# Optimization experiments

Measured on AMD Instinct MI355X. Metric: run time of the kernel, lower is better.

The kernel has to match this reference:

```python
import jax, jax.numpy as jnp
import numpy as np

N_NODES = 100_000
N_EDGES = 3_200_000
D_FEAT = 64


def setup_inputs() -> dict:
    key = jax.random.key(0)
    k1, k2, k3, k4, k5 = jax.random.split(key, 5)
    x = jax.random.normal(k1, (N_EDGES, D_FEAT), dtype=jnp.float32)
    switch = jax.random.uniform(k2, (N_EDGES,), dtype=jnp.float32)
    edge_src = jax.random.randint(k3, (N_EDGES,), 0, N_NODES, dtype=jnp.int32)
    edge_dst = jax.random.randint(k4, (N_EDGES,), 0, N_NODES, dtype=jnp.int32)
    species = jax.random.randint(k5, (N_NODES,), 0, 90, dtype=jnp.int32)
    return {"x": x, "switch": switch, "edge_src": edge_src,
            "edge_dst": edge_dst, "species": species}


def reference(x, switch, edge_src, edge_dst, species):
    # nat = inputs['species'].shape[0]  (static under jit)
    nat = species.shape[0]
    # apply_switch: gate each edge feature row by its scalar switch value
    xg = x * switch[:, None]                      # [E, D]
    # undirected graph: scatter-add into both endpoints
    out = jax.ops.segment_sum(xg, edge_src, num_segments=nat)
    out = out + jax.ops.segment_sum(xg, edge_dst, num_segments=nat)
    return out                                     # [nat, D]
```

## Files before the change

### kernel.cpp

```cpp
#include <hip/hip_runtime.h>


#define D_FEAT 64
#define EPB 8192
#define KMAX 1024
#define BCAP 24576

__global__ __launch_bounds__(256) void scatter_edges_atomic_kernel(
    const float4* __restrict__ x, const float* __restrict__ sw,
    const int* __restrict__ src, const int* __restrict__ dst,
    float* __restrict__ out, int n_edges)
{
    long long tid = (long long)blockIdx.x * blockDim.x + threadIdx.x;
    long long total = (long long)n_edges * 16;
    if (tid >= total) return;
    int e = (int)(tid >> 4);
    int q = (int)(tid & 15);
    float s = sw[e];
    float4 v = x[(long long)e * 16 + q];
    v.x *= s; v.y *= s; v.z *= s; v.w *= s;
    float* oa = out + (long long)src[e] * D_FEAT + q * 4;
    float* ob = out + (long long)dst[e] * D_FEAT + q * 4;
    unsafeAtomicAdd(oa + 0, v.x); unsafeAtomicAdd(oa + 1, v.y);
    unsafeAtomicAdd(oa + 2, v.z); unsafeAtomicAdd(oa + 3, v.w);
    unsafeAtomicAdd(ob + 0, v.x); unsafeAtomicAdd(ob + 1, v.y);
    unsafeAtomicAdd(ob + 2, v.z); unsafeAtomicAdd(ob + 3, v.w);
}

__global__ __launch_bounds__(512) void bucket_hist_kernel(
    const int* __restrict__ src, const int* __restrict__ dst,
    int* __restrict__ bsize, int n_edges, int K)
{
    __shared__ int h[KMAX];
    for (int j = threadIdx.x; j < K; j += 512) h[j] = 0;
    __syncthreads();
    int base = blockIdx.x * EPB;
    int m = min(EPB, n_edges - base);
    for (int i = threadIdx.x; i < m; i += 512) {
        int s = src[base + i], d = dst[base + i];
        atomicAdd(&h[s >> 8], 1);
        atomicAdd(&h[d >> 8], 1);
    }
    __syncthreads();
    for (int j = threadIdx.x; j < K; j += 512)
        if (h[j]) atomicAdd(&bsize[j], h[j]);
}

__global__ __launch_bounds__(1024) void bucket_scan_kernel(
    const int* __restrict__ bsize, int* __restrict__ bbase,
    int* __restrict__ bcursor, int K)
{
    __shared__ int s[KMAX + 1];
    int t = threadIdx.x;
    if (t < K) s[t] = bsize[t];
    __syncthreads();
    if (t == 0) {
        int a = 0;
        for (int j = 0; j < K; ++j) { int v = s[j]; s[j] = a; a += v; }
        s[K] = a;
    }
    __syncthreads();
    if (t <= K) bbase[t] = s[t];
    if (t < K)  bcursor[t] = s[t];
}

__global__ __launch_bounds__(512) void partition_kernel(
    const int* __restrict__ src, const int* __restrict__ dst,
    int* __restrict__ bcursor, unsigned int* __restrict__ pe, int n_edges)
{
    __shared__ int ebs[EPB];
    __shared__ int ebd[EPB];
    __shared__ int cnt[KMAX];
    __shared__ int cur[KMAX];
    for (int j = threadIdx.x; j < KMAX; j += 512) cnt[j] = 0;
    __syncthreads();
    int base = blockIdx.x * EPB;
    int m = min(EPB, n_edges - base);
    for (int i = threadIdx.x; i < m; i += 512) {
        int s = src[base + i], d = dst[base + i];
        ebs[i] = s; ebd[i] = d;
        atomicAdd(&cnt[s >> 8], 1);
        atomicAdd(&cnt[d >> 8], 1);
    }
    __syncthreads();
    for (int j = threadIdx.x; j < KMAX; j += 512) {
        int c = cnt[j];
        cur[j] = c ? atomicAdd(&bcursor[j], c) : 0;
    }
    __syncthreads();
    for (int i = threadIdx.x; i < m; i += 512) {
        unsigned int e = (unsigned int)(base + i);
        int s = ebs[i], d = ebd[i];
        int ps = atomicAdd(&cur[s >> 8], 1);
        pe[ps] = ((unsigned int)(s & 255) << 24) | e;
        int pd = atomicAdd(&cur[d >> 8], 1);
        pe[pd] = ((unsigned int)(d & 255) << 24) | e;
    }
}

__global__ __launch_bounds__(512) void bucket_sort_kernel(
    const int* __restrict__ bbase, unsigned int* __restrict__ pe,
    int* __restrict__ offs_g, int* __restrict__ counts_g, int n_nodes)
{
    __shared__ unsigned int ent[BCAP];
    __shared__ int cnt[256];
    __shared__ int cur[256];
    int k = blockIdx.x;
    int base = bbase[k];
    int m = bbase[k + 1] - base;
    for (int j = threadIdx.x; j < 256; j += 512) cnt[j] = 0;
    __syncthreads();
    for (int i = threadIdx.x; i < m; i += 512) {
        unsigned int v = pe[base + i];
        ent[i] = v;
        atomicAdd(&cnt[v >> 24], 1);
    }
    __syncthreads();
    if (threadIdx.x == 0) {
        int a = 0;
        for (int j = 0; j < 256; ++j) { int c = cnt[j]; cur[j] = a; a += c; }
    }
    __syncthreads();
    for (int j = threadIdx.x; j < 256; j += 512) {
        int lo = cur[j];
        int n = (k << 8) + j;
        if (n < n_nodes) { counts_g[n] = cnt[j]; offs_g[n] = base + lo; }
        cur[j] = base + lo;
    }
    __syncthreads();
    for (int i = threadIdx.x; i < m; i += 512) {
        unsigned int v = ent[i];
        int pos = atomicAdd(&cur[v >> 24], 1);
        pe[pos] = v;
    }
}

__global__ __launch_bounds__(256) void gather_kernel(
    const float* __restrict__ x, const float* __restrict__ sw,
    const int* __restrict__ offs_g, const int* __restrict__ counts_g,
    const unsigned int* __restrict__ pe, float* __restrict__ out, int n_nodes)
{
    int wave = blockIdx.x * 4 + (threadIdx.x >> 6);
    int lane = threadIdx.x & 63;
    if (wave >= n_nodes) return;
    int start = offs_g[wave];
    int cnt = counts_g[wave];

    float acc = 0.0f;
    int i = 0;
    for (; i + 8 <= cnt; i += 8) {
        int e0 = (int)(pe[start + i + 0] & 0x3FFFFFu);
        int e1 = (int)(pe[start + i + 1] & 0x3FFFFFu);
        int e2 = (int)(pe[start + i + 2] & 0x3FFFFFu);
        int e3 = (int)(pe[start + i + 3] & 0x3FFFFFu);
        int e4 = (int)(pe[start + i + 4] & 0x3FFFFFu);
        int e5 = (int)(pe[start + i + 5] & 0x3FFFFFu);
        int e6 = (int)(pe[start + i + 6] & 0x3FFFFFu);
        int e7 = (int)(pe[start + i + 7] & 0x3FFFFFu);
        float v0 = __builtin_nontemporal_load(x + (long long)e0 * D_FEAT + lane);
        float v1 = __builtin_nontemporal_load(x + (long long)e1 * D_FEAT + lane);
        float v2 = __builtin_nontemporal_load(x + (long long)e2 * D_FEAT + lane);
        float v3 = __builtin_nontemporal_load(x + (long long)e3 * D_FEAT + lane);
        float v4 = __builtin_nontemporal_load(x + (long long)e4 * D_FEAT + lane);
        float v5 = __builtin_nontemporal_load(x + (long long)e5 * D_FEAT + lane);
        float v6 = __builtin_nontemporal_load(x + (long long)e6 * D_FEAT + lane);
        float v7 = __builtin_nontemporal_load(x + (long long)e7 * D_FEAT + lane);
        float s0 = sw[e0], s1 = sw[e1], s2 = sw[e2], s3 = sw[e3];
        float s4 = sw[e4], s5 = sw[e5], s6 = sw[e6], s7 = sw[e7];
        acc += v0 * s0; acc += v1 * s1; acc += v2 * s2; acc += v3 * s3;
        acc += v4 * s4; acc += v5 * s5; acc += v6 * s6; acc += v7 * s7;
    }
    for (; i < cnt; ++i) {
        int e = (int)(pe[start + i] & 0x3FFFFFu);
        acc += __builtin_nontemporal_load(x + (long long)e * D_FEAT + lane) * sw[e];
    }
    out[(long long)wave * D_FEAT + lane] = acc;
}

extern "C" void kernel_launch(void* const* d_in, const int* in_sizes, int n_in,
                              void* d_out, int out_size, void* d_ws, size_t ws_size,
                              hipStream_t stream) {
    const float* x   = (const float*)d_in[0];
    const float* sw  = (const float*)d_in[1];
    const int*   src = (const int*)d_in[2];
    const int*   dst = (const int*)d_in[3];
    float* out = (float*)d_out;

    int n_edges = in_sizes[1];
    int n_nodes = in_sizes[4];

    int K = (n_nodes + 255) >> 8;

    char* wsb = (char*)d_ws;
    size_t off = 0;
    int* bsize   = (int*)(wsb + off); off += (size_t)K * 4;
    int* bbase   = (int*)(wsb + off); off += (size_t)(K + 1) * 4;
    int* bcursor = (int*)(wsb + off); off += (size_t)K * 4;
    int* offs_g  = (int*)(wsb + off); off += (size_t)n_nodes * 4;
    int* cnts_g  = (int*)(wsb + off); off += (size_t)n_nodes * 4;
    off = (off + 255) & ~(size_t)255;
    unsigned int* pe = (unsigned int*)(wsb + off);
    off += (size_t)n_edges * 2 * 4;
    size_t needed = off;

    long long avg_per_bucket = (2LL * n_edges) / (K > 0 ? K : 1);
    bool fast_ok = (K >= 1) && (K <= KMAX)
                && (n_edges > 0) && (n_edges < (1 << 22))
                && (avg_per_bucket <= 20000)
                && (ws_size >= needed);

    if (!fast_ok) {
        hipMemsetAsync(d_out, 0, (size_t)out_size * sizeof(float), stream);
        long long total = (long long)n_edges * 16;
        int block = 256;
        long long grid = (total + block - 1) / block;
        scatter_edges_atomic_kernel<<<(int)grid, block, 0, stream>>>(
            (const float4*)x, sw, src, dst, out, n_edges);
        return;
    }

    int nblkE = (n_edges + EPB - 1) / EPB;

    hipMemsetAsync(bsize, 0, (size_t)K * 4, stream);

    bucket_hist_kernel<<<nblkE, 512, 0, stream>>>(src, dst, bsize, n_edges, K);
    bucket_scan_kernel<<<1, 1024, 0, stream>>>(bsize, bbase, bcursor, K);
    partition_kernel<<<nblkE, 512, 0, stream>>>(src, dst, bcursor, pe, n_edges);
    bucket_sort_kernel<<<K, 512, 0, stream>>>(bbase, pe, offs_g, cnts_g, n_nodes);

    int gblk = (n_nodes + 3) / 4;
    gather_kernel<<<gblk, 256, 0, stream>>>(x, sw, offs_g, cnts_g, pe, out, n_nodes);
}
```

Baseline: 477.1 us.

## Use 128-node buckets, parallel scans, and float4 gather with four edges per wave

Bucket size drops from 256 to 128 nodes, so K is 782 and each bucket sort holds fewer entries, which means less shared memory per block and more blocks. The serial single-thread scans in the bucket scan and bucket sort kernels become Hillis-Steele parallel scans. The partition kernel no longer stages src/dst in shared memory and re-reads them from global instead. The gather kernel now processes four edges per wave, each 16-lane group loading a full 256B row as float4 and combining results with xor shuffles. The bucket sort clamps its entry count to BCAP, which could silently drop edges if a bucket overflows.

```diff
diff --git a/kernel.cpp b/kernel.cpp
--- a/kernel.cpp
+++ b/kernel.cpp
@@ -4,7 +4,10 @@
 #define D_FEAT 64
 #define EPB 8192
 #define KMAX 1024
-#define BCAP 24576
+#define BNODES 128
+#define BCAP 12288
+
+typedef float f32x4 __attribute__((ext_vector_type(4)));
 
 __global__ __launch_bounds__(256) void scatter_edges_atomic_kernel(
     const float4* __restrict__ x, const float* __restrict__ sw,
@@ -37,64 +40,63 @@
     int base = blockIdx.x * EPB;
     int m = min(EPB, n_edges - base);
     for (int i = threadIdx.x; i < m; i += 512) {
-        int s = src[base + i], d = dst[base + i];
-        atomicAdd(&h[s >> 8], 1);
-        atomicAdd(&h[d >> 8], 1);
+        atomicAdd(&h[src[base + i] >> 7], 1);
+        atomicAdd(&h[dst[base + i] >> 7], 1);
     }
     __syncthreads();
     for (int j = threadIdx.x; j < K; j += 512)
         if (h[j]) atomicAdd(&bsize[j], h[j]);
 }
 
-__global__ __launch_bounds__(1024) void bucket_scan_kernel(
+__global__ __launch_bounds__(KMAX) void bucket_scan_kernel(
     const int* __restrict__ bsize, int* __restrict__ bbase,
     int* __restrict__ bcursor, int K)
 {
-    __shared__ int s[KMAX + 1];
+    __shared__ int s[KMAX];
     int t = threadIdx.x;
-    if (t < K) s[t] = bsize[t];
-    __syncthreads();
-    if (t == 0) {
-        int a = 0;
-        for (int j = 0; j < K; ++j) { int v = s[j]; s[j] = a; a += v; }
-        s[K] = a;
-    }
-    __syncthreads();
-    if (t <= K) bbase[t] = s[t];
-    if (t < K)  bcursor[t] = s[t];
+    int v = (t < K) ? bsize[t] : 0;
+    int acc = v;
+    s[t] = acc;
+    __syncthreads();
+    for (int d = 1; d < KMAX; d <<= 1) {
+        int add = (t >= d) ? s[t - d] : 0;
+        __syncthreads();
+        acc += add;
+        s[t] = acc;
+        __syncthreads();
+    }
+    if (t < K) { int ex = acc - v; bbase[t] = ex; bcursor[t] = ex; }
+    if (t == K - 1) bbase[K] = acc;
 }
 
 __global__ __launch_bounds__(512) void partition_kernel(
     const int* __restrict__ src, const int* __restrict__ dst,
-    int* __restrict__ bcursor, unsigned int* __restrict__ pe, int n_edges)
-{
-    __shared__ int ebs[EPB];
-    __shared__ int ebd[EPB];
+    int* __restrict__ bcursor, unsigned int* __restrict__ pe,
+    int n_edges, int K)
+{
     __shared__ int cnt[KMAX];
     __shared__ int cur[KMAX];
-    for (int j = threadIdx.x; j < KMAX; j += 512) cnt[j] = 0;
+    for (int j = threadIdx.x; j < K; j += 512) cnt[j] = 0;
     __syncthreads();
     int base = blockIdx.x * EPB;
     int m = min(EPB, n_edges - base);
     for (int i = threadIdx.x; i < m; i += 512) {
-        int s = src[base + i], d = dst[base + i];
-        ebs[i] = s; ebd[i] = d;
-        atomicAdd(&cnt[s >> 8], 1);
-        atomicAdd(&cnt[d >> 8], 1);
-    }
-    __syncthreads();
-    for (int j = threadIdx.x; j < KMAX; j += 512) {
+        atomicAdd(&cnt[src[base + i] >> 7], 1);
+        atomicAdd(&cnt[dst[base + i] >> 7], 1);
+    }
+    __syncthreads();
+    for (int j = threadIdx.x; j < K; j += 512) {
         int c = cnt[j];
         cur[j] = c ? atomicAdd(&bcursor[j], c) : 0;
     }
     __syncthreads();
     for (int i = threadIdx.x; i < m; i += 512) {
+        int s = src[base + i], d = dst[base + i];
         unsigned int e = (unsigned int)(base + i);
-        int s = ebs[i], d = ebd[i];
-        int ps = atomicAdd(&cur[s >> 8], 1);
-        pe[ps] = ((unsigned int)(s & 255) << 24) | e;
-        int pd = atomicAdd(&cur[d >> 8], 1);
-        pe[pd] = ((unsigned int)(d & 255) << 24) | e;
+        int ps = atomicAdd(&cur[s >> 7], 1);
+        pe[ps] = ((unsigned int)(s & 127) << 24) | e;
+        int pd = atomicAdd(&cur[d >> 7], 1);
+        pe[pd] = ((unsigned int)(d & 127) << 24) | e;
     }
 }
 
@@ -103,78 +105,96 @@
     int* __restrict__ offs_g, int* __restrict__ counts_g, int n_nodes)
 {
     __shared__ unsigned int ent[BCAP];
-    __shared__ int cnt[256];
-    __shared__ int cur[256];
+    __shared__ int cnt[BNODES];
+    __shared__ int cur[BNODES];
     int k = blockIdx.x;
+    int t = threadIdx.x;
     int base = bbase[k];
     int m = bbase[k + 1] - base;
-    for (int j = threadIdx.x; j < 256; j += 512) cnt[j] = 0;
-    __syncthreads();
-    for (int i = threadIdx.x; i < m; i += 512) {
+    if (m > BCAP) m = BCAP;
+    if (t < BNODES) cnt[t] = 0;
+    __syncthreads();
+    for (int i = t; i < m; i += 512) {
         unsigned int v = pe[base + i];
         ent[i] = v;
-        atomicAdd(&cnt[v >> 24], 1);
-    }
-    __syncthreads();
-    if (threadIdx.x == 0) {
-        int a = 0;
-        for (int j = 0; j < 256; ++j) { int c = cnt[j]; cur[j] = a; a += c; }
-    }
-    __syncthreads();
-    for (int j = threadIdx.x; j < 256; j += 512) {
-        int lo = cur[j];
-        int n = (k << 8) + j;
-        if (n < n_nodes) { counts_g[n] = cnt[j]; offs_g[n] = base + lo; }
-        cur[j] = base + lo;
-    }
-    __syncthreads();
-    for (int i = threadIdx.x; i < m; i += 512) {
+        atomicAdd(&cnt[(v >> 24) & 127], 1);
+    }
+    __syncthreads();
+    int v0 = 0, acc = 0;
+    if (t < BNODES) { v0 = cnt[t]; acc = v0; cur[t] = acc; }
+    __syncthreads();
+    for (int d = 1; d < BNODES; d <<= 1) {
+        int add = 0;
+        if (t < BNODES && t >= d) add = cur[t - d];
+        __syncthreads();
+        if (t < BNODES) { acc += add; cur[t] = acc; }
+        __syncthreads();
+    }
+    if (t < BNODES) {
+        int ex = acc - v0;
+        int n = (k << 7) + t;
+        if (n < n_nodes) { counts_g[n] = v0; offs_g[n] = base + ex; }
+        cur[t] = base + ex;
+    }
+    __syncthreads();
+    for (int i = t; i < m; i += 512) {
         unsigned int v = ent[i];
-        int pos = atomicAdd(&cur[v >> 24], 1);
+        int pos = atomicAdd(&cur[(v >> 24) & 127], 1);
         pe[pos] = v;
     }
 }
 
 __global__ __launch_bounds__(256) void gather_kernel(
-    const float* __restrict__ x, const float* __restrict__ sw,
+    const f32x4* __restrict__ x4, const float* __restrict__ sw,
     const int* __restrict__ offs_g, const int* __restrict__ counts_g,
-    const unsigned int* __restrict__ pe, float* __restrict__ out, int n_nodes)
+    const unsigned int* __restrict__ pe, f32x4* __restrict__ out4,
+    int n_nodes)
 {
     int wave = blockIdx.x * 4 + (threadIdx.x >> 6);
     int lane = threadIdx.x & 63;
     if (wave >= n_nodes) return;
     int start = offs_g[wave];
     int cnt = counts_g[wave];
-
-    float acc = 0.0f;
+    int cl = lane >> 4;
+    int fq = lane & 15;
+
+    f32x4 acc = {0.f, 0.f, 0.f, 0.f};
     int i = 0;
-    for (; i + 8 <= cnt; i += 8) {
-        int e0 = (int)(pe[start + i + 0] & 0x3FFFFFu);
-        int e1 = (int)(pe[start + i + 1] & 0x3FFFFFu);
-        int e2 = (int)(pe[start + i + 2] & 0x3FFFFFu);
-        int e3 = (int)(pe[start + i + 3] & 0x3FFFFFu);
-        int e4 = (int)(pe[start + i + 4] & 0x3FFFFFu);
-        int e5 = (int)(pe[start + i + 5] & 0x3FFFFFu);
-        int e6 = (int)(pe[start + i + 6] & 0x3FFFFFu);
-        int e7 = (int)(pe[start + i + 7] & 0x3FFFFFu);
-        float v0 = __builtin_nontemporal_load(x + (long long)e0 * D_FEAT + lane);
-        float v1 = __builtin_nontemporal_load(x + (long long)e1 * D_FEAT + lane);
-        float v2 = __builtin_nontemporal_load(x + (long long)e2 * D_FEAT + lane);
-        float v3 = __builtin_nontemporal_load(x + (long long)e3 * D_FEAT + lane);
-        float v4 = __builtin_nontemporal_load(x + (long long)e4 * D_FEAT + lane);
-        float v5 = __builtin_nontemporal_load(x + (long long)e5 * D_FEAT + lane);
-        float v6 = __builtin_nontemporal_load(x + (long long)e6 * D_FEAT + lane);
-        float v7 = __builtin_nontemporal_load(x + (long long)e7 * D_FEAT + lane);
+    for (; i + 16 <= cnt; i += 16) {
+        int j = start + i + cl;
+        unsigned int p0 = pe[j];
+        unsigned int p1 = pe[j + 4];
+        unsigned int p2 = pe[j + 8];
+        unsigned int p3 = pe[j + 12];
+        int e0 = (int)(p0 & 0x3FFFFFu);
+        int e1 = (int)(p1 & 0x3FFFFFu);
+        int e2 = (int)(p2 & 0x3FFFFFu);
+        int e3 = (int)(p3 & 0x3FFFFFu);
+        f32x4 v0 = __builtin_nontemporal_load(x4 + (long long)e0 * 16 + fq);
+        f32x4 v1 = __builtin_nontemporal_load(x4 + (long long)e1 * 16 + fq);
+        f32x4 v2 = __builtin_nontemporal_load(x4 + (long long)e2 * 16 + fq);
+        f32x4 v3 = __builtin_nontemporal_load(x4 + (long long)e3 * 16 + fq);
         float s0 = sw[e0], s1 = sw[e1], s2 = sw[e2], s3 = sw[e3];
-        float s4 = sw[e4], s5 = sw[e5], s6 = sw[e6], s7 = sw[e7];
         acc += v0 * s0; acc += v1 * s1; acc += v2 * s2; acc += v3 * s3;
-        acc += v4 * s4; acc += v5 * s5; acc += v6 * s6; acc += v7 * s7;
-    }
-    for (; i < cnt; ++i) {
-        int e = (int)(pe[start + i] & 0x3FFFFFu);
-        acc += __builtin_nontemporal_load(x + (long long)e * D_FEAT + lane) * sw[e];
-    }
-    out[(long long)wave * D_FEAT + lane] = acc;
+    }
+    for (; i < cnt; i += 4) {
+        int j = i + cl;
+        if (j < cnt) {
+            unsigned int p = pe[start + j];
+            int e = (int)(p & 0x3FFFFFu);
+            f32x4 v = __builtin_nontemporal_load(x4 + (long long)e * 16 + fq);
+            acc += v * sw[e];
+        }
+    }
+    acc.x += __shfl_xor(acc.x, 16, 64);
+    acc.y += __shfl_xor(acc.y, 16, 64);
+    acc.z += __shfl_xor(acc.z, 16, 64);
+    acc.w += __shfl_xor(acc.w, 16, 64);
+    acc.x += __shfl_xor(acc.x, 32, 64);
+    acc.y += __shfl_xor(acc.y, 32, 64);
+    acc.z += __shfl_xor(acc.z, 32, 64);
+    acc.w += __shfl_xor(acc.w, 32, 64);
+    if (cl == 0) out4[(long long)wave * 16 + fq] = acc;
 }
 
 extern "C" void kernel_launch(void* const* d_in, const int* in_sizes, int n_in,
@@ -189,13 +209,14 @@
     int n_edges = in_sizes[1];
     int n_nodes = in_sizes[4];
 
-    int K = (n_nodes + 255) >> 8;
+    int K = (n_nodes + BNODES - 1) >> 7;
 
     char* wsb = (char*)d_ws;
     size_t off = 0;
     int* bsize   = (int*)(wsb + off); off += (size_t)K * 4;
     int* bbase   = (int*)(wsb + off); off += (size_t)(K + 1) * 4;
     int* bcursor = (int*)(wsb + off); off += (size_t)K * 4;
+    off = (off + 255) & ~(size_t)255;
     int* offs_g  = (int*)(wsb + off); off += (size_t)n_nodes * 4;
     int* cnts_g  = (int*)(wsb + off); off += (size_t)n_nodes * 4;
     off = (off + 255) & ~(size_t)255;
@@ -206,7 +227,7 @@
     long long avg_per_bucket = (2LL * n_edges) / (K > 0 ? K : 1);
     bool fast_ok = (K >= 1) && (K <= KMAX)
                 && (n_edges > 0) && (n_edges < (1 << 22))
-                && (avg_per_bucket <= 20000)
+                && (avg_per_bucket <= 10000)
                 && (ws_size >= needed);
 
     if (!fast_ok) {
@@ -224,10 +245,11 @@
     hipMemsetAsync(bsize, 0, (size_t)K * 4, stream);
 
     bucket_hist_kernel<<<nblkE, 512, 0, stream>>>(src, dst, bsize, n_edges, K);
-    bucket_scan_kernel<<<1, 1024, 0, stream>>>(bsize, bbase, bcursor, K);
-    partition_kernel<<<nblkE, 512, 0, stream>>>(src, dst, bcursor, pe, n_edges);
+    bucket_scan_kernel<<<1, KMAX, 0, stream>>>(bsize, bbase, bcursor, K);
+    partition_kernel<<<nblkE, 512, 0, stream>>>(src, dst, bcursor, pe, n_edges, K);
     bucket_sort_kernel<<<K, 512, 0, stream>>>(bbase, pe, offs_g, cnts_g, n_nodes);
 
     int gblk = (n_nodes + 3) / 4;
-    gather_kernel<<<gblk, 256, 0, stream>>>(x, sw, offs_g, cnts_g, pe, out, n_nodes);
-}
+    gather_kernel<<<gblk, 256, 0, stream>>>(
+        (const f32x4*)x, sw, offs_g, cnts_g, pe, (f32x4*)out, n_nodes);
+}
```

New measurement: 462.7 us. 3.0% less time.
